# Kernel tuning notes

Hardware: AMD Instinct MI355X
Metric: run time of the kernel (lower is better)

## Reference

```python
import jax, jax.numpy as jnp
import numpy as np

EPS = 1e-6

def setup_inputs() -> dict:
    key = jax.random.key(0)
    k1, k2, k3, k4 = jax.random.split(key, 4)
    B, N, E, C_in, C_out = 8, 4096, 2048, 128, 128
    x = jax.random.normal(k1, (B, N, C_in), dtype=jnp.float32)
    H = jax.random.uniform(k2, (B, N, E), dtype=jnp.float32)
    # nn.Linear(in_ch, out_ch): W is [out_ch, in_ch], b is [out_ch]
    W = jax.random.normal(k3, (C_out, C_in), dtype=jnp.float32) / np.sqrt(C_in)
    b = jax.random.normal(k4, (C_out,), dtype=jnp.float32) * 0.01
    return {"x": x, "H": H, "W": W, "b": b}

def reference(x, H, W, b):
    # Degree normalizers (diag_embed + bmm in original == broadcast row scale)
    De = jnp.sum(H, axis=1) + EPS          # [B, E] hyperedge degrees
    Dv = jnp.sum(H, axis=2) + EPS          # [B, N] node degrees
    inv_sqrt_Dv = 1.0 / jnp.sqrt(Dv)       # [B, N]
    out = x * inv_sqrt_Dv[..., None]                 # Dv^{-1/2} x
    out = jnp.einsum('bne,bnc->bec', H, out)         # H^T (..)
    out = out / De[..., None]                        # De^{-1} (..)
    out = jnp.einsum('bne,bec->bnc', H, out)         # H (..)
    out = out * inv_sqrt_Dv[..., None]               # Dv^{-1/2} (..)
    return out @ W.T + b                             # Linear
```

## Files before the change

kernel.cpp:

```cpp
#include <hip/hip_runtime.h>


#define EPS 1e-6f
constexpr int B_ = 8, N_ = 4096, E_ = 2048, C_ = 128;

typedef __bf16 bf16x8 __attribute__((ext_vector_type(8)));
typedef float f32x4 __attribute__((ext_vector_type(4)));

__device__ __forceinline__ unsigned int f2bf_pack(float lo, float hi) {
  unsigned int ul = __float_as_uint(lo), uh = __float_as_uint(hi);
  ul = (ul + 0x7fffu + ((ul >> 16) & 1u)) >> 16;
  uh = (uh + 0x7fffu + ((uh >> 16) & 1u)) & 0xffff0000u;
  return uh | ul;
}

__device__ __forceinline__ void gl2lds16(const void* g, void* l) {
  __builtin_amdgcn_global_load_lds(
      (const __attribute__((address_space(1))) void*)g,
      (__attribute__((address_space(3))) void*)l, 16, 0, 0);
}

__global__ __launch_bounds__(256) void k1_prep(
    const float* __restrict__ H, unsigned short* __restrict__ Hbf,
    unsigned short* __restrict__ HT, float* __restrict__ Dv, float* __restrict__ De) {
  __shared__ float T[64][129];
  const int t = threadIdx.x;
  const int b = blockIdx.z;
  const int n0 = blockIdx.x * 128;
  const int ebase = blockIdx.y * 1024;
  const int nloc = t >> 1, eh = t & 1;
  const int erow = t >> 2, nq = t & 3;
  const float* Hrow = H + ((size_t)b * N_ + n0 + nloc) * E_;
  unsigned short* HbfRow = Hbf + ((size_t)b * N_ + n0 + nloc) * E_;
  float rowsum = 0.f;
  for (int ch = 0; ch < 16; ++ch) {
    const int e0 = ebase + ch * 64;
    const int eoff = e0 + eh * 32;
    f32x4 v[8];
    const f32x4* src = (const f32x4*)(Hrow + eoff);
#pragma unroll
    for (int i = 0; i < 8; ++i) v[i] = src[i];
    unsigned int pk[16];
#pragma unroll
    for (int i = 0; i < 8; ++i) {
      rowsum += v[i][0] + v[i][1] + v[i][2] + v[i][3];
      pk[2 * i] = f2bf_pack(v[i][0], v[i][1]);
      pk[2 * i + 1] = f2bf_pack(v[i][2], v[i][3]);
    }
    uint4* dst = (uint4*)(HbfRow + eoff);
#pragma unroll
    for (int i = 0; i < 4; ++i)
      dst[i] = make_uint4(pk[4 * i], pk[4 * i + 1], pk[4 * i + 2], pk[4 * i + 3]);
    __syncthreads();
#pragma unroll
    for (int i = 0; i < 8; ++i) {
      const int el = eh * 32 + 4 * i;
      T[el + 0][nloc] = v[i][0];
      T[el + 1][nloc] = v[i][1];
      T[el + 2][nloc] = v[i][2];
      T[el + 3][nloc] = v[i][3];
    }
    __syncthreads();
    float csum = 0.f;
    unsigned int hp[16];
#pragma unroll
    for (int i = 0; i < 16; ++i) {
      const float a0 = T[erow][nq * 32 + 2 * i];
      const float a1 = T[erow][nq * 32 + 2 * i + 1];
      csum += a0 + a1;
      hp[i] = f2bf_pack(a0, a1);
    }
    uint4* hdst = (uint4*)(HT + ((size_t)b * E_ + e0 + erow) * N_ + n0 + nq * 32);
#pragma unroll
    for (int i = 0; i < 4; ++i)
      hdst[i] = make_uint4(hp[4 * i], hp[4 * i + 1], hp[4 * i + 2], hp[4 * i + 3]);
    csum += __shfl_down(csum, 1);
    csum += __shfl_down(csum, 2);
    if ((t & 3) == 0) atomicAdd(&De[b * E_ + e0 + erow], csum);
  }
  rowsum += __shfl_down(rowsum, 1);
  if (eh == 0) atomicAdd(&Dv[b * N_ + n0 + nloc], rowsum);
}

template <int MODE>
__global__ __launch_bounds__(256) void scale_transpose(
    const float* __restrict__ in, const float* __restrict__ deg,
    unsigned short* __restrict__ outT, int R) {
  __shared__ unsigned int T[128][66];
  const int t = threadIdx.x;
  in += (size_t)blockIdx.y * R * 128;
  outT += (size_t)blockIdx.y * 128 * R;
  deg += (size_t)blockIdx.y * R;
  const int r0 = blockIdx.x * 128;
  const int q = t >> 2, cq = t & 3;
  const float* row0 = in + (size_t)(r0 + 2 * q) * 128;
  const float* row1 = row0 + 128;
  const float d0 = deg[r0 + 2 * q] + EPS, d1 = deg[r0 + 2 * q + 1] + EPS;
  float s0, s1;
  if (MODE == 0) { s0 = 1.f / sqrtf(d0); s1 = 1.f / sqrtf(d1); }
  else { s0 = 1.f / d0; s1 = 1.f / d1; }
#pragma unroll
  for (int i = 0; i < 8; ++i) {
    const int c = 16 * i + 4 * cq;
    const f32x4 a = *(const f32x4*)(row0 + c);
    const f32x4 b2 = *(const f32x4*)(row1 + c);
#pragma unroll
    for (int j = 0; j < 4; ++j) T[c + j][q] = f2bf_pack(a[j] * s0, b2[j] * s1);
  }
  __syncthreads();
  const int crow = t >> 1, h = t & 1;
  unsigned int u[32];
#pragma unroll
  for (int i = 0; i < 32; ++i) u[i] = T[crow][h * 32 + i];
  uint4* dst = (uint4*)(outT + (size_t)crow * R + r0 + 64 * h);
#pragma unroll
  for (int i = 0; i < 8; ++i)
    dst[i] = make_uint4(u[4 * i], u[4 * i + 1], u[4 * i + 2], u[4 * i + 3]);
}

__global__ __launch_bounds__(256) void gemm_bt_splitk(
    const unsigned short* __restrict__ A, const unsigned short* __restrict__ Bt,
    float* __restrict__ Cacc, int M, int Kfull, int Kper) {
  __shared__ unsigned short Als[128 * 32];
  __shared__ unsigned short Bls[128 * 32];
  const int t = threadIdx.x;
  const int w = t >> 6, l = t & 63;
  const int mt = blockIdx.x, sk = blockIdx.y, b = blockIdx.z;
  const unsigned short* Ab = A + ((size_t)b * M + mt * 128) * Kfull + (size_t)sk * Kper;
  const unsigned short* Btb = Bt + (size_t)b * 128 * Kfull + (size_t)sk * Kper;
  const int srow = l >> 2, scol = (l & 3) * 8;
  const unsigned short* ga0 = Ab + (size_t)(w * 32 + srow) * Kfull + scol;
  const unsigned short* ga1 = ga0 + (size_t)16 * Kfull;
  const unsigned short* gb0 = Btb + (size_t)(w * 32 + srow) * Kfull + scol;
  const unsigned short* gb1 = gb0 + (size_t)16 * Kfull;
  unsigned short* const la0 = Als + (w * 32) * 32;
  unsigned short* const la1 = Als + (w * 32 + 16) * 32;
  unsigned short* const lb0 = Bls + (w * 32) * 32;
  unsigned short* const lb1 = Bls + (w * 32 + 16) * 32;
  const int mrow = (w & 1) * 64, ncol = (w >> 1) * 64;
  const int fr = l & 15, fq = l >> 4;
  f32x4 acc[4][4];
#pragma unroll
  for (int i = 0; i < 4; ++i)
#pragma unroll
    for (int j = 0; j < 4; ++j) acc[i][j] = (f32x4){0.f, 0.f, 0.f, 0.f};
  const int nsteps = Kper / 32;
  for (int kt = 0; kt < nsteps; ++kt) {
    __syncthreads();
    gl2lds16(ga0, la0);
    gl2lds16(ga1, la1);
    gl2lds16(gb0, lb0);
    gl2lds16(gb1, lb1);
    ga0 += 32; ga1 += 32; gb0 += 32; gb1 += 32;
    __syncthreads();
    bf16x8 af[4], bfr[4];
#pragma unroll
    for (int i = 0; i < 4; ++i) {
      af[i] = *(const bf16x8*)(Als + (mrow + i * 16 + fr) * 32 + fq * 8);
      bfr[i] = *(const bf16x8*)(Bls + (ncol + i * 16 + fr) * 32 + fq * 8);
    }
#pragma unroll
    for (int i = 0; i < 4; ++i)
#pragma unroll
      for (int j = 0; j < 4; ++j)
        acc[i][j] = __builtin_amdgcn_mfma_f32_16x16x32_bf16(af[i], bfr[j], acc[i][j], 0, 0, 0);
  }
  float* Cb = Cacc + ((size_t)b * M + mt * 128) * 128;
#pragma unroll
  for (int i = 0; i < 4; ++i)
#pragma unroll
    for (int j = 0; j < 4; ++j)
#pragma unroll
      for (int r = 0; r < 4; ++r) {
        const int row = mrow + i * 16 + fq * 4 + r;
        const int col = ncol + j * 16 + fr;
        atomicAdd(Cb + (size_t)row * 128 + col, acc[i][j][r]);
      }
}

__global__ __launch_bounds__(256) void k5_linear(
    float* __restrict__ io, const float* __restrict__ W,
    const float* __restrict__ bias, const float* __restrict__ Dv) {
  __shared__ unsigned short Als[128 * 136];
  __shared__ unsigned short Wls[128 * 136];
  const int t = threadIdx.x;
  const size_t r0 = (size_t)blockIdx.x * 128;
  {
    const int row = t >> 1, h = t & 1;
    const float* src = io + (r0 + row) * 128 + h * 64;
    const float sc = 1.f / sqrtf(Dv[r0 + row] + EPS);
    unsigned short* ld = Als + row * 136 + h * 64;
    const float* wsrc = W + row * 128 + h * 64;
    unsigned short* lw = Wls + row * 136 + h * 64;
#pragma unroll
    for (int i = 0; i < 16; ++i) {
      const f32x4 a = *(const f32x4*)(src + 4 * i);
      uint2 p;
      p.x = f2bf_pack(a[0] * sc, a[1] * sc);
      p.y = f2bf_pack(a[2] * sc, a[3] * sc);
      *(uint2*)(ld + 4 * i) = p;
      const f32x4 ww = *(const f32x4*)(wsrc + 4 * i);
      uint2 pw;
      pw.x = f2bf_pack(ww[0], ww[1]);
      pw.y = f2bf_pack(ww[2], ww[3]);
      *(uint2*)(lw + 4 * i) = pw;
    }
  }
  __syncthreads();
  const int w = t >> 6, l = t & 63;
  const int mrow = (w & 1) * 64, ncol = (w >> 1) * 64;
  const int fr = l & 15, fq = l >> 4;
  f32x4 acc[4][4];
#pragma unroll
  for (int i = 0; i < 4; ++i)
#pragma unroll
    for (int j = 0; j < 4; ++j) acc[i][j] = (f32x4){0.f, 0.f, 0.f, 0.f};
#pragma unroll
  for (int s = 0; s < 4; ++s) {
    bf16x8 af[4], bfr[4];
#pragma unroll
    for (int i = 0; i < 4; ++i) {
      af[i] = *(const bf16x8*)(Als + (mrow + i * 16 + fr) * 136 + s * 32 + fq * 8);
      bfr[i] = *(const bf16x8*)(Wls + (ncol + i * 16 + fr) * 136 + s * 32 + fq * 8);
    }
#pragma unroll
    for (int i = 0; i < 4; ++i)
#pragma unroll
      for (int j = 0; j < 4; ++j)
        acc[i][j] = __builtin_amdgcn_mfma_f32_16x16x32_bf16(af[i], bfr[j], acc[i][j], 0, 0, 0);
  }
#pragma unroll
  for (int i = 0; i < 4; ++i)
#pragma unroll
    for (int j = 0; j < 4; ++j)
#pragma unroll
      for (int r = 0; r < 4; ++r) {
        const int row = mrow + i * 16 + fq * 4 + r;
        const int col = ncol + j * 16 + fr;
        io[(r0 + row) * 128 + col] = acc[i][j][r] + bias[col];
      }
}

extern "C" void kernel_launch(void* const* d_in, const int* in_sizes, int n_in,
                              void* d_out, int out_size, void* d_ws, size_t ws_size,
                              hipStream_t stream) {
  const float* x = (const float*)d_in[0];
  const float* H = (const float*)d_in[1];
  const float* W = (const float*)d_in[2];
  const float* bias = (const float*)d_in[3];
  float* out = (float*)d_out;

  char* ws = (char*)d_ws;
  unsigned short* Hbf = (unsigned short*)ws;
  unsigned short* HT = Hbf + (size_t)B_ * N_ * E_;
  unsigned short* xsT = HT + (size_t)B_ * N_ * E_;
  float* out2 = (float*)(xsT + (size_t)B_ * C_ * N_);
  unsigned short* out2T = (unsigned short*)(out2 + (size_t)B_ * E_ * C_);
  float* Dv = (float*)(out2T + (size_t)B_ * C_ * E_);
  float* De = Dv + B_ * N_;

  hipMemsetAsync(Dv, 0, (size_t)(B_ * N_ + B_ * E_) * sizeof(float), stream);
  hipMemsetAsync(out2, 0, (size_t)B_ * E_ * C_ * sizeof(float), stream);
  hipMemsetAsync(d_out, 0, (size_t)out_size * sizeof(float), stream);

  k1_prep<<<dim3(N_ / 128, E_ / 1024, B_), 256, 0, stream>>>(H, Hbf, HT, Dv, De);
  scale_transpose<0><<<dim3(N_ / 128, B_), 256, 0, stream>>>(x, Dv, xsT, N_);
  gemm_bt_splitk<<<dim3(E_ / 128, 4, B_), 256, 0, stream>>>(HT, xsT, out2, E_, N_, N_ / 4);
  scale_transpose<1><<<dim3(E_ / 128, B_), 256, 0, stream>>>(out2, De, out2T, E_);
  gemm_bt_splitk<<<dim3(N_ / 128, 2, B_), 256, 0, stream>>>(Hbf, out2T, out, N_, E_, E_ / 2);
  k5_linear<<<dim3(B_ * N_ / 128), 256, 0, stream>>>(out, W, bias, Dv);
}
```

Measured before the change: 596.5 us.

## Split H prep into cast and bf16 transpose; replace split-K atomics with partial buffers

The fused H prep kernel is split in two. One kernel casts H to bf16 and computes node degrees with one wave per row. A second kernel transposes the bf16 copy to build HT and accumulates edge degrees. The split-K GEMMs now write plain stores into two separate partial buffers instead of using float atomicAdd. The downstream scale/transpose and linear kernels sum the two partials, which removes two memsets and the atomic traffic. The first GEMM uses split-K of 2 instead of 4. Buffers are reused across stages (output and HT memory as scratch) to fit the workspace. In exchange, H is read again in bf16 for the transpose, De is now computed from bf16-rounded values, and there is one more kernel launch.

```diff
diff --git a/kernel.cpp b/kernel.cpp
--- a/kernel.cpp
+++ b/kernel.cpp
@@ -20,85 +20,80 @@
       (__attribute__((address_space(3))) void*)l, 16, 0, 0);
 }
 
-__global__ __launch_bounds__(256) void k1_prep(
+__global__ __launch_bounds__(256) void k1a_cast_dv(
     const float* __restrict__ H, unsigned short* __restrict__ Hbf,
-    unsigned short* __restrict__ HT, float* __restrict__ Dv, float* __restrict__ De) {
-  __shared__ float T[64][129];
+    float* __restrict__ Dv) {
+  const int t = threadIdx.x;
+  const int w = t >> 6, l = t & 63;
+  const size_t row = (size_t)blockIdx.x * 4 + w;
+  const float* src = H + row * E_;
+  unsigned short* dst = Hbf + row * E_;
+  float s = 0.f;
+#pragma unroll
+  for (int i = 0; i < 8; ++i) {
+    const f32x4 v = *(const f32x4*)(src + 256 * i + 4 * l);
+    s += v[0] + v[1] + v[2] + v[3];
+    uint2 p;
+    p.x = f2bf_pack(v[0], v[1]);
+    p.y = f2bf_pack(v[2], v[3]);
+    *(uint2*)(dst + 256 * i + 4 * l) = p;
+  }
+#pragma unroll
+  for (int o = 32; o; o >>= 1) s += __shfl_xor(s, o);
+  if (l == 0) Dv[row] = s;
+}
+
+__global__ __launch_bounds__(256) void k1b_transpose_de(
+    const unsigned short* __restrict__ Hbf, unsigned short* __restrict__ HT,
+    float* __restrict__ De) {
+  __shared__ unsigned int T[128][66];
   const int t = threadIdx.x;
   const int b = blockIdx.z;
-  const int n0 = blockIdx.x * 128;
-  const int ebase = blockIdx.y * 1024;
-  const int nloc = t >> 1, eh = t & 1;
-  const int erow = t >> 2, nq = t & 3;
-  const float* Hrow = H + ((size_t)b * N_ + n0 + nloc) * E_;
-  unsigned short* HbfRow = Hbf + ((size_t)b * N_ + n0 + nloc) * E_;
-  float rowsum = 0.f;
-  for (int ch = 0; ch < 16; ++ch) {
-    const int e0 = ebase + ch * 64;
-    const int eoff = e0 + eh * 32;
-    f32x4 v[8];
-    const f32x4* src = (const f32x4*)(Hrow + eoff);
-#pragma unroll
-    for (int i = 0; i < 8; ++i) v[i] = src[i];
-    unsigned int pk[16];
-#pragma unroll
-    for (int i = 0; i < 8; ++i) {
-      rowsum += v[i][0] + v[i][1] + v[i][2] + v[i][3];
-      pk[2 * i] = f2bf_pack(v[i][0], v[i][1]);
-      pk[2 * i + 1] = f2bf_pack(v[i][2], v[i][3]);
-    }
-    uint4* dst = (uint4*)(HbfRow + eoff);
-#pragma unroll
-    for (int i = 0; i < 4; ++i)
-      dst[i] = make_uint4(pk[4 * i], pk[4 * i + 1], pk[4 * i + 2], pk[4 * i + 3]);
-    __syncthreads();
-#pragma unroll
-    for (int i = 0; i < 8; ++i) {
-      const int el = eh * 32 + 4 * i;
-      T[el + 0][nloc] = v[i][0];
-      T[el + 1][nloc] = v[i][1];
-      T[el + 2][nloc] = v[i][2];
-      T[el + 3][nloc] = v[i][3];
-    }
-    __syncthreads();
-    float csum = 0.f;
-    unsigned int hp[16];
-#pragma unroll
-    for (int i = 0; i < 16; ++i) {
-      const float a0 = T[erow][nq * 32 + 2 * i];
-      const float a1 = T[erow][nq * 32 + 2 * i + 1];
-      csum += a0 + a1;
-      hp[i] = f2bf_pack(a0, a1);
-    }
-    uint4* hdst = (uint4*)(HT + ((size_t)b * E_ + e0 + erow) * N_ + n0 + nq * 32);
-#pragma unroll
-    for (int i = 0; i < 4; ++i)
-      hdst[i] = make_uint4(hp[4 * i], hp[4 * i + 1], hp[4 * i + 2], hp[4 * i + 3]);
-    csum += __shfl_down(csum, 1);
-    csum += __shfl_down(csum, 2);
-    if ((t & 3) == 0) atomicAdd(&De[b * E_ + e0 + erow], csum);
-  }
-  rowsum += __shfl_down(rowsum, 1);
-  if (eh == 0) atomicAdd(&Dv[b * N_ + n0 + nloc], rowsum);
-}
-
-template <int MODE>
-__global__ __launch_bounds__(256) void scale_transpose(
+  const int n0 = blockIdx.x * 128, e0 = blockIdx.y * 128;
+  const int q = t >> 2, cq = t & 3;
+  const unsigned short* r0p = Hbf + ((size_t)b * N_ + n0 + 2 * q) * E_ + e0;
+  const unsigned short* r1p = r0p + E_;
+#pragma unroll
+  for (int i = 0; i < 8; ++i) {
+    const int c = 16 * i + 4 * cq;
+    const uint2 a = *(const uint2*)(r0p + c);
+    const uint2 bb = *(const uint2*)(r1p + c);
+    T[c + 0][q] = (a.x & 0xffffu) | (bb.x << 16);
+    T[c + 1][q] = (a.x >> 16) | (bb.x & 0xffff0000u);
+    T[c + 2][q] = (a.y & 0xffffu) | (bb.y << 16);
+    T[c + 3][q] = (a.y >> 16) | (bb.y & 0xffff0000u);
+  }
+  __syncthreads();
+  const int crow = t >> 1, h = t & 1;
+  unsigned int u[32];
+  float s = 0.f;
+#pragma unroll
+  for (int i = 0; i < 32; ++i) {
+    u[i] = T[crow][h * 32 + i];
+    s += __uint_as_float(u[i] << 16) + __uint_as_float(u[i] & 0xffff0000u);
+  }
+  uint4* dst = (uint4*)(HT + ((size_t)b * E_ + e0 + crow) * N_ + n0 + 64 * h);
+#pragma unroll
+  for (int i = 0; i < 8; ++i)
+    dst[i] = make_uint4(u[4 * i], u[4 * i + 1], u[4 * i + 2], u[4 * i + 3]);
+  s += __shfl_xor(s, 1);
+  if (h == 0) atomicAdd(&De[b * E_ + e0 + crow], s);
+}
+
+__global__ __launch_bounds__(256) void st0_scale_transpose(
     const float* __restrict__ in, const float* __restrict__ deg,
-    unsigned short* __restrict__ outT, int R) {
+    unsigned short* __restrict__ outT) {
   __shared__ unsigned int T[128][66];
   const int t = threadIdx.x;
-  in += (size_t)blockIdx.y * R * 128;
-  outT += (size_t)blockIdx.y * 128 * R;
-  deg += (size_t)blockIdx.y * R;
+  in += (size_t)blockIdx.y * N_ * 128;
+  outT += (size_t)blockIdx.y * 128 * N_;
+  deg += (size_t)blockIdx.y * N_;
   const int r0 = blockIdx.x * 128;
   const int q = t >> 2, cq = t & 3;
   const float* row0 = in + (size_t)(r0 + 2 * q) * 128;
   const float* row1 = row0 + 128;
-  const float d0 = deg[r0 + 2 * q] + EPS, d1 = deg[r0 + 2 * q + 1] + EPS;
-  float s0, s1;
-  if (MODE == 0) { s0 = 1.f / sqrtf(d0); s1 = 1.f / sqrtf(d1); }
-  else { s0 = 1.f / d0; s1 = 1.f / d1; }
+  const float s0 = 1.f / sqrtf(deg[r0 + 2 * q] + EPS);
+  const float s1 = 1.f / sqrtf(deg[r0 + 2 * q + 1] + EPS);
 #pragma unroll
   for (int i = 0; i < 8; ++i) {
     const int c = 16 * i + 4 * cq;
@@ -112,15 +107,48 @@
   unsigned int u[32];
 #pragma unroll
   for (int i = 0; i < 32; ++i) u[i] = T[crow][h * 32 + i];
-  uint4* dst = (uint4*)(outT + (size_t)crow * R + r0 + 64 * h);
+  uint4* dst = (uint4*)(outT + (size_t)crow * N_ + r0 + 64 * h);
 #pragma unroll
   for (int i = 0; i < 8; ++i)
     dst[i] = make_uint4(u[4 * i], u[4 * i + 1], u[4 * i + 2], u[4 * i + 3]);
 }
 
+__global__ __launch_bounds__(256) void st1_sum(
+    const float* __restrict__ p0, const float* __restrict__ p1,
+    const float* __restrict__ De, unsigned short* __restrict__ out2T) {
+  __shared__ unsigned int T[128][66];
+  const int t = threadIdx.x;
+  const int b = blockIdx.y;
+  const int r0 = blockIdx.x * 128;
+  const int q = t >> 2, cq = t & 3;
+  const size_t base = ((size_t)b * E_ + r0 + 2 * q) * C_;
+  const float s0 = 1.f / (De[b * E_ + r0 + 2 * q] + EPS);
+  const float s1 = 1.f / (De[b * E_ + r0 + 2 * q + 1] + EPS);
+#pragma unroll
+  for (int i = 0; i < 8; ++i) {
+    const int c = 16 * i + 4 * cq;
+    const f32x4 a = *(const f32x4*)(p0 + base + c);
+    const f32x4 a1 = *(const f32x4*)(p1 + base + c);
+    const f32x4 bb = *(const f32x4*)(p0 + base + C_ + c);
+    const f32x4 b1 = *(const f32x4*)(p1 + base + C_ + c);
+#pragma unroll
+    for (int j = 0; j < 4; ++j)
+      T[c + j][q] = f2bf_pack((a[j] + a1[j]) * s0, (bb[j] + b1[j]) * s1);
+  }
+  __syncthreads();
+  const int crow = t >> 1, h = t & 1;
+  unsigned int u[32];
+#pragma unroll
+  for (int i = 0; i < 32; ++i) u[i] = T[crow][h * 32 + i];
+  uint4* dst = (uint4*)(out2T + ((size_t)b * C_ + crow) * E_ + r0 + 64 * h);
+#pragma unroll
+  for (int i = 0; i < 8; ++i)
+    dst[i] = make_uint4(u[4 * i], u[4 * i + 1], u[4 * i + 2], u[4 * i + 3]);
+}
+
 __global__ __launch_bounds__(256) void gemm_bt_splitk(
     const unsigned short* __restrict__ A, const unsigned short* __restrict__ Bt,
-    float* __restrict__ Cacc, int M, int Kfull, int Kper) {
+    float* __restrict__ C0, float* __restrict__ C1, int M, int Kfull, int Kper) {
   __shared__ unsigned short Als[128 * 32];
   __shared__ unsigned short Bls[128 * 32];
   const int t = threadIdx.x;
@@ -165,7 +193,7 @@
       for (int j = 0; j < 4; ++j)
         acc[i][j] = __builtin_amdgcn_mfma_f32_16x16x32_bf16(af[i], bfr[j], acc[i][j], 0, 0, 0);
   }
-  float* Cb = Cacc + ((size_t)b * M + mt * 128) * 128;
+  float* Cb = (sk == 0 ? C0 : C1) + ((size_t)b * M + mt * 128) * 128;
 #pragma unroll
   for (int i = 0; i < 4; ++i)
 #pragma unroll
@@ -174,30 +202,33 @@
       for (int r = 0; r < 4; ++r) {
         const int row = mrow + i * 16 + fq * 4 + r;
         const int col = ncol + j * 16 + fr;
-        atomicAdd(Cb + (size_t)row * 128 + col, acc[i][j][r]);
+        Cb[(size_t)row * 128 + col] = acc[i][j][r];
       }
 }
 
 __global__ __launch_bounds__(256) void k5_linear(
-    float* __restrict__ io, const float* __restrict__ W,
-    const float* __restrict__ bias, const float* __restrict__ Dv) {
+    float* __restrict__ io, const float* __restrict__ q1,
+    const float* __restrict__ W, const float* __restrict__ bias,
+    const float* __restrict__ Dv) {
   __shared__ unsigned short Als[128 * 136];
   __shared__ unsigned short Wls[128 * 136];
   const int t = threadIdx.x;
   const size_t r0 = (size_t)blockIdx.x * 128;
   {
     const int row = t >> 1, h = t & 1;
-    const float* src = io + (r0 + row) * 128 + h * 64;
+    const float* src0 = io + (r0 + row) * 128 + h * 64;
+    const float* src1 = q1 + (r0 + row) * 128 + h * 64;
     const float sc = 1.f / sqrtf(Dv[r0 + row] + EPS);
     unsigned short* ld = Als + row * 136 + h * 64;
     const float* wsrc = W + row * 128 + h * 64;
     unsigned short* lw = Wls + row * 136 + h * 64;
 #pragma unroll
     for (int i = 0; i < 16; ++i) {
-      const f32x4 a = *(const f32x4*)(src + 4 * i);
+      const f32x4 a = *(const f32x4*)(src0 + 4 * i);
+      const f32x4 a1 = *(const f32x4*)(src1 + 4 * i);
       uint2 p;
-      p.x = f2bf_pack(a[0] * sc, a[1] * sc);
-      p.y = f2bf_pack(a[2] * sc, a[3] * sc);
+      p.x = f2bf_pack((a[0] + a1[0]) * sc, (a[1] + a1[1]) * sc);
+      p.y = f2bf_pack((a[2] + a1[2]) * sc, (a[3] + a1[3]) * sc);
       *(uint2*)(ld + 4 * i) = p;
       const f32x4 ww = *(const f32x4*)(wsrc + 4 * i);
       uint2 pw;
@@ -250,23 +281,24 @@
   const float* bias = (const float*)d_in[3];
   float* out = (float*)d_out;
 
-  char* ws = (char*)d_ws;
-  unsigned short* Hbf = (unsigned short*)ws;
+  unsigned short* Hbf = (unsigned short*)d_ws;
   unsigned short* HT = Hbf + (size_t)B_ * N_ * E_;
   unsigned short* xsT = HT + (size_t)B_ * N_ * E_;
-  float* out2 = (float*)(xsT + (size_t)B_ * C_ * N_);
-  unsigned short* out2T = (unsigned short*)(out2 + (size_t)B_ * E_ * C_);
+  unsigned short* out2T = xsT + (size_t)B_ * C_ * N_;
   float* Dv = (float*)(out2T + (size_t)B_ * C_ * E_);
   float* De = Dv + B_ * N_;
 
-  hipMemsetAsync(Dv, 0, (size_t)(B_ * N_ + B_ * E_) * sizeof(float), stream);
-  hipMemsetAsync(out2, 0, (size_t)B_ * E_ * C_ * sizeof(float), stream);
-  hipMemsetAsync(d_out, 0, (size_t)out_size * sizeof(float), stream);
-
-  k1_prep<<<dim3(N_ / 128, E_ / 1024, B_), 256, 0, stream>>>(H, Hbf, HT, Dv, De);
-  scale_transpose<0><<<dim3(N_ / 128, B_), 256, 0, stream>>>(x, Dv, xsT, N_);
-  gemm_bt_splitk<<<dim3(E_ / 128, 4, B_), 256, 0, stream>>>(HT, xsT, out2, E_, N_, N_ / 4);
-  scale_transpose<1><<<dim3(E_ / 128, B_), 256, 0, stream>>>(out2, De, out2T, E_);
-  gemm_bt_splitk<<<dim3(N_ / 128, 2, B_), 256, 0, stream>>>(Hbf, out2T, out, N_, E_, E_ / 2);
-  k5_linear<<<dim3(B_ * N_ / 128), 256, 0, stream>>>(out, W, bias, Dv);
-}
+  float* g1p0 = out;
+  float* g1p1 = out + (size_t)B_ * E_ * C_;
+  float* g2p1 = (float*)HT;
+
+  hipMemsetAsync(De, 0, (size_t)B_ * E_ * sizeof(float), stream);
+
+  k1a_cast_dv<<<dim3(B_ * N_ / 4), 256, 0, stream>>>(H, Hbf, Dv);
+  k1b_transpose_de<<<dim3(N_ / 128, E_ / 128, B_), 256, 0, stream>>>(Hbf, HT, De);
+  st0_scale_transpose<<<dim3(N_ / 128, B_), 256, 0, stream>>>(x, Dv, xsT);
+  gemm_bt_splitk<<<dim3(E_ / 128, 2, B_), 256, 0, stream>>>(HT, xsT, g1p0, g1p1, E_, N_, N_ / 2);
+  st1_sum<<<dim3(E_ / 128, B_), 256, 0, stream>>>(g1p0, g1p1, De, out2T);
+  gemm_bt_splitk<<<dim3(N_ / 128, 2, B_), 256, 0, stream>>>(Hbf, out2T, out, g2p1, N_, E_, E_ / 2);
+  k5_linear<<<dim3(B_ * N_ / 128), 256, 0, stream>>>(out, g2p1, W, bias, Dv);
+}
```

New measurement: 592.5 us. No clear change (-0.7%).
